# Performance work log

Hardware: AMD Instinct MI355X
Metric: run time of the kernel (lower is better)

The kernel has to match this reference:

```python
import jax, jax.numpy as jnp
import numpy as np

N_FULL = 50000
N_POOL = 12500
E_FULL = 600000
E_POOL = 150000
D = 128


def gcn_conv(x, W, b, edge_index, n):
    """GCNConv with self-loops and symmetric normalization.
    x: [n, d_in], W: [d_in, d_out], edge_index: [2, E] (src -> dst)."""
    xw = x @ W  # [n, d_out]
    loops = jnp.arange(n, dtype=edge_index.dtype)
    src = jnp.concatenate([edge_index[0], loops])
    dst = jnp.concatenate([edge_index[1], loops])
    deg = jnp.zeros((n,), dtype=xw.dtype).at[dst].add(1.0)  # >= 1 (self loops)
    dinv = jax.lax.rsqrt(deg)
    norm = (dinv[src] * dinv[dst])[:, None]  # [E+n, 1]
    out = jax.ops.segment_sum(xw[src] * norm, dst, num_segments=n)
    return out + b


def setup_inputs() -> dict:
    key = jax.random.key(0)
    ks = jax.random.split(key, 8)
    s = 1.0 / np.sqrt(D)
    return {
        "x": jnp.zeros((N_FULL, D), jnp.float32),
        "edge_index": jax.random.randint(ks[0], (2, E_FULL), 0, N_FULL, dtype=jnp.int64)
            if jax.config.jax_enable_x64 else jax.random.randint(ks[0], (2, E_FULL), 0, N_FULL).astype(jnp.int32),
        "pooled_x": jax.random.normal(ks[1], (N_POOL, D), jnp.float32),
        "pooled_edge_index": jax.random.randint(ks[2], (2, E_POOL), 0, N_POOL).astype(jnp.int32),
        "unpool_info": jnp.arange(N_POOL, dtype=jnp.int32),  # unique TopK-kept indices
        "W0": jax.random.normal(ks[3], (D, D), jnp.float32) * s,
        "b0": jnp.zeros((D,), jnp.float32),
        "W1": jax.random.normal(ks[4], (D, D), jnp.float32) * s,
        "b1": jnp.zeros((D,), jnp.float32),
        "W2": jax.random.normal(ks[5], (D, D), jnp.float32) * s,
        "b2": jnp.zeros((D,), jnp.float32),
    }


def reference(x, edge_index, pooled_x, pooled_edge_index, unpool_info,
              W0, b0, W1, b1, W2, b2):
    n = x.shape[0]
    # conv0 on the pooled graph + activation (ELU)
    h = jax.nn.elu(gcn_conv(pooled_x, W0, b0, pooled_edge_index, pooled_x.shape[0]))
    # TopKPool unpool: zero full graph, scatter pooled features to kept indices
    xf = jnp.zeros_like(x).at[unpool_info].set(h)
    # remaining convs on the full graph (dropout=0 / eval mode -> identity)
    xf = jax.nn.elu(gcn_conv(xf, W1, b1, edge_index, n))
    xf = jax.nn.elu(gcn_conv(xf, W2, b2, edge_index, n))
    return xf
```

## Files before the change

### kernel.cpp

```cpp
#include <hip/hip_runtime.h>
#include <math.h>

#define DD 128

static inline int cdiv(long a, long b){ return (int)((a + b - 1) / b); }

__device__ __forceinline__ unsigned bfpack(float a, float b){
  unsigned ua = __float_as_uint(a), ub = __float_as_uint(b);
  ua = (ua + 0x7fffu + ((ua >> 16) & 1u)) >> 16;
  ub = (ub + 0x7fffu + ((ub >> 16) & 1u)) >> 16;
  return ua | (ub << 16);
}

__global__ void k_count2(const int* __restrict__ dst_f, int Ef, int* __restrict__ cnt_f,
                         int* __restrict__ rank_f,
                         const int* __restrict__ dst_p, int Ep, int* __restrict__ cnt_p,
                         int* __restrict__ rank_p,
                         int* __restrict__ invm, int nf){
  int e = blockIdx.x * blockDim.x + threadIdx.x;
  if (e < Ef){ rank_f[e] = atomicAdd(&cnt_f[dst_f[e]], 1); return; }
  e -= Ef;
  if (e < Ep){ rank_p[e] = atomicAdd(&cnt_p[dst_p[e]], 1); return; }
  e -= Ep;
  if (e < nf) invm[e] = -1;
}

__global__ __launch_bounds__(256) void k_bsum(
    const int* __restrict__ cnt_f, int nf, const int* __restrict__ cnt_p, int np,
    int* __restrict__ bsum_f, int* __restrict__ bsum_p, int nbf, int nbp,
    const int* __restrict__ unpool, int* __restrict__ inv, int npool){
  int bi = blockIdx.x;
  if (bi >= nbf + nbp){
    int i = (bi - nbf - nbp) * 256 + threadIdx.x;
    if (i < npool) inv[unpool[i]] = i;
    return;
  }
  const int* cnt; int n; int* bsum; int b;
  if (bi < nbf){ cnt = cnt_f; n = nf; bsum = bsum_f; b = bi; }
  else         { cnt = cnt_p; n = np; bsum = bsum_p; b = bi - nbf; }
  __shared__ int s[256];
  int t = threadIdx.x;
  long base = (long)b * 1024 + t * 4;
  int v = 0;
  if (base + 3 < n){ int4 q = *(const int4*)(cnt + base); v = q.x + q.y + q.z + q.w; }
  else { for (int j = 0; j < 4; j++) if (base + j < n) v += cnt[base + j]; }
  s[t] = v; __syncthreads();
  for (int off = 128; off > 0; off >>= 1){ if (t < off) s[t] += s[t + off]; __syncthreads(); }
  if (t == 0) bsum[b] = s[0];
}

__global__ __launch_bounds__(128) void k_scan_b(int* __restrict__ bsum_f, int nbf,
                                                int* __restrict__ bsum_p, int nbp){
  __shared__ int s[128];
  int t = threadIdx.x;
  int v = (t < nbf) ? bsum_f[t] : 0;
  s[t] = v; __syncthreads();
  for (int off = 1; off < 128; off <<= 1){ int u = (t >= off) ? s[t - off] : 0; __syncthreads(); s[t] += u; __syncthreads(); }
  if (t < nbf) bsum_f[t] = s[t] - v;
  __syncthreads();
  int v2 = (t < nbp) ? bsum_p[t] : 0;
  s[t] = v2; __syncthreads();
  for (int off = 1; off < 128; off <<= 1){ int u = (t >= off) ? s[t - off] : 0; __syncthreads(); s[t] += u; __syncthreads(); }
  if (t < nbp) bsum_p[t] = s[t] - v2;
}

__global__ __launch_bounds__(256) void k_scan_f(
    const int* __restrict__ cnt_f, int nf, const int* __restrict__ bsum_f,
    const int* __restrict__ cnt_p, int np, const int* __restrict__ bsum_p,
    int* __restrict__ rptr_f, float* __restrict__ dinv_f,
    int* __restrict__ rptr_p, float* __restrict__ dinv_p,
    int nbf, int Ef, int Ep){
  const int* cnt; const int* bsum; int* rptr; float* dinv; int n; int b;
  if ((int)blockIdx.x < nbf){ cnt=cnt_f; bsum=bsum_f; rptr=rptr_f; dinv=dinv_f; n=nf; b=blockIdx.x; }
  else                      { cnt=cnt_p; bsum=bsum_p; rptr=rptr_p; dinv=dinv_p; n=np; b=blockIdx.x-nbf; }
  __shared__ int s[256];
  int t = threadIdx.x;
  long base = (long)b * 1024 + t * 4;
  int c0=0,c1=0,c2=0,c3=0;
  if (base + 3 < n){ int4 q = *(const int4*)(cnt + base); c0=q.x; c1=q.y; c2=q.z; c3=q.w; }
  else {
    if (base + 0 < n) c0 = cnt[base + 0];
    if (base + 1 < n) c1 = cnt[base + 1];
    if (base + 2 < n) c2 = cnt[base + 2];
  }
  int tsum = c0 + c1 + c2 + c3;
  s[t] = tsum; __syncthreads();
  for (int off = 1; off < 256; off <<= 1){ int u = (t >= off) ? s[t - off] : 0; __syncthreads(); s[t] += u; __syncthreads(); }
  int run = bsum[b] + s[t] - tsum;
  int r0 = run, r1 = r0 + c0, r2 = r1 + c1, r3 = r2 + c2;
  if (base + 3 < n){
    *(int4*)(rptr + base) = make_int4(r0, r1, r2, r3);
    dinv[base + 0] = rsqrtf((float)(c0 + 1));
    dinv[base + 1] = rsqrtf((float)(c1 + 1));
    dinv[base + 2] = rsqrtf((float)(c2 + 1));
    dinv[base + 3] = rsqrtf((float)(c3 + 1));
  } else {
    if (base + 0 < n){ rptr[base+0]=r0; dinv[base+0]=rsqrtf((float)(c0+1)); }
    if (base + 1 < n){ rptr[base+1]=r1; dinv[base+1]=rsqrtf((float)(c1+1)); }
    if (base + 2 < n){ rptr[base+2]=r2; dinv[base+2]=rsqrtf((float)(c2+1)); }
  }
  if (blockIdx.x == 0 && t == 0){ rptr_f[nf] = Ef; rptr_p[np] = Ep; }
}

__global__ void k_fill2(const int* __restrict__ src_f, const int* __restrict__ dst_f, int Ef,
                        const int* __restrict__ rptr_f, const int* __restrict__ rank_f,
                        int4* __restrict__ ewk_f,
                        const float* __restrict__ dinv_f, const int* __restrict__ inv,
                        const int* __restrict__ src_p, const int* __restrict__ dst_p, int Ep,
                        const int* __restrict__ rptr_p, const int* __restrict__ rank_p,
                        int2* __restrict__ ewk_p,
                        const float* __restrict__ dinv_p){
  int e = blockIdx.x * blockDim.x + threadIdx.x;
  if (e < Ef){
    int s = src_f[e];
    int p = rptr_f[dst_f[e]] + rank_f[e];
    ewk_f[p] = make_int4(s, inv[s], __float_as_int(dinv_f[s]), 0);
  } else {
    e -= Ef;
    if (e < Ep){
      int s = src_p[e];
      int p = rptr_p[dst_p[e]] + rank_p[e];
      ewk_p[p] = make_int2(s, __float_as_int(dinv_p[s]));
    }
  }
}

template <bool BF16OUT>
__global__ __launch_bounds__(256) void k_gemm_t(const float* __restrict__ A,
                                                const float* __restrict__ W,
                                                void* __restrict__ Cout, int n){
  __shared__ float As[16][132];
  __shared__ float Ws[16][128];
  const int t    = threadIdx.x;
  const int row0 = blockIdx.x * 128;
  const int tc   = t & 15;
  const int tr   = t >> 4;
  const int sr   = t >> 2;
  const int sq   = (t & 3) * 4;
  const int wr   = t >> 4;
  const int wq   = (t & 15) * 4;

  float acc[8][8];
  #pragma unroll
  for (int i = 0; i < 8; i++)
    #pragma unroll
    for (int j = 0; j < 8; j++) acc[i][j] = 0.f;

  for (int kt = 0; kt < 128; kt += 16){
    float4 a0 = make_float4(0.f,0.f,0.f,0.f), a1 = a0;
    int r0 = row0 + sr, r1 = row0 + sr + 64;
    if (r0 < n) a0 = *(const float4*)(A + (long)r0 * DD + kt + sq);
    if (r1 < n) a1 = *(const float4*)(A + (long)r1 * DD + kt + sq);
    const float4 wv0 = *(const float4*)(W + (long)(kt + wr) * DD + wq);
    const float4 wv1 = *(const float4*)(W + (long)(kt + wr) * DD + wq + 64);
    __syncthreads();
    As[sq + 0][sr]      = a0.x;  As[sq + 1][sr]      = a0.y;
    As[sq + 2][sr]      = a0.z;  As[sq + 3][sr]      = a0.w;
    As[sq + 0][sr + 64] = a1.x;  As[sq + 1][sr + 64] = a1.y;
    As[sq + 2][sr + 64] = a1.z;  As[sq + 3][sr + 64] = a1.w;
    *(float4*)(&Ws[wr][wq])      = wv0;
    *(float4*)(&Ws[wr][wq + 64]) = wv1;
    __syncthreads();
    #pragma unroll
    for (int k = 0; k < 16; k++){
      const float4 af0 = *(const float4*)(&As[k][tr * 8]);
      const float4 af1 = *(const float4*)(&As[k][tr * 8 + 4]);
      const float4 wf0 = *(const float4*)(&Ws[k][tc * 8]);
      const float4 wf1 = *(const float4*)(&Ws[k][tc * 8 + 4]);
      const float ar[8] = {af0.x,af0.y,af0.z,af0.w,af1.x,af1.y,af1.z,af1.w};
      const float wv[8] = {wf0.x,wf0.y,wf0.z,wf0.w,wf1.x,wf1.y,wf1.z,wf1.w};
      #pragma unroll
      for (int i = 0; i < 8; i++)
        #pragma unroll
        for (int j = 0; j < 8; j++)
          acc[i][j] += ar[i] * wv[j];
    }
  }
  if (BF16OUT){
    unsigned short* C = (unsigned short*)Cout;
    #pragma unroll
    for (int i = 0; i < 8; i++){
      int row = row0 + tr * 8 + i;
      if (row < n){
        uint4 pk;
        pk.x = bfpack(acc[i][0], acc[i][1]);
        pk.y = bfpack(acc[i][2], acc[i][3]);
        pk.z = bfpack(acc[i][4], acc[i][5]);
        pk.w = bfpack(acc[i][6], acc[i][7]);
        *(uint4*)(C + (long)row * DD + tc * 8) = pk;
      }
    }
  } else {
    float* C = (float*)Cout;
    #pragma unroll
    for (int i = 0; i < 8; i++){
      int row = row0 + tr * 8 + i;
      if (row < n){
        *(float4*)(C + (long)row * DD + tc * 8)     = make_float4(acc[i][0], acc[i][1], acc[i][2], acc[i][3]);
        *(float4*)(C + (long)row * DD + tc * 8 + 4) = make_float4(acc[i][4], acc[i][5], acc[i][6], acc[i][7]);
      }
    }
  }
}

__global__ __launch_bounds__(256) void k_agg_csr(const float* __restrict__ xw,
    const int* __restrict__ rptr, const int2* __restrict__ ewk,
    const float* __restrict__ dinv, const float* __restrict__ b,
    float* __restrict__ out, int n){
  int row = blockIdx.x * 4 + (threadIdx.x >> 6);
  if (row >= n) return;
  int c = (threadIdx.x & 63) * 2;
  int j0 = __builtin_amdgcn_readfirstlane(rptr[row]);
  int j1 = __builtin_amdgcn_readfirstlane(rptr[row + 1]);
  float ax[4], ay[4];
  #pragma unroll
  for (int i = 0; i < 4; i++){ ax[i] = 0.f; ay[i] = 0.f; }
  int j = j0;
  for (; j + 3 < j1; j += 4){
    #pragma unroll
    for (int i = 0; i < 4; i++){
      int2 q = ewk[j + i];
      float w = __int_as_float(q.y);
      float2 v = *(const float2*)(xw + (long)q.x * DD + c);
      ax[i] += v.x * w; ay[i] += v.y * w;
    }
  }
  for (; j < j1; j++){
    int2 q = ewk[j];
    float w = __int_as_float(q.y);
    float2 v = *(const float2*)(xw + (long)q.x * DD + c);
    ax[0] += v.x * w; ay[0] += v.y * w;
  }
  float sax = (ax[0]+ax[1]) + (ax[2]+ax[3]);
  float say = (ay[0]+ay[1]) + (ay[2]+ay[3]);
  float dd = dinv[row];
  float2 sv = *(const float2*)(xw + (long)row * DD + c);
  float2 bb = *(const float2*)(b + c);
  float vx = sax * dd + sv.x * dd * dd + bb.x;
  float vy = say * dd + sv.y * dd * dd + bb.y;
  vx = vx > 0.f ? vx : expm1f(vx);
  vy = vy > 0.f ? vy : expm1f(vy);
  *(float2*)(out + (long)row * DD + c) = make_float2(vx, vy);
}

__global__ __launch_bounds__(256) void k_agg_csr_b(const unsigned short* __restrict__ xwb,
    const int* __restrict__ rptr, const int4* __restrict__ ewk,
    const float* __restrict__ dinv, const float* __restrict__ b,
    float* __restrict__ out, int n){
  int row = blockIdx.x * 4 + (threadIdx.x >> 6);
  if (row >= n) return;
  int c = (threadIdx.x & 63) * 2;
  int j0 = __builtin_amdgcn_readfirstlane(rptr[row]);
  int j1 = __builtin_amdgcn_readfirstlane(rptr[row + 1]);
  float ax[8], ay[8];
  #pragma unroll
  for (int i = 0; i < 8; i++){ ax[i] = 0.f; ay[i] = 0.f; }
  int j = j0;
  for (; j + 7 < j1; j += 8){
    #pragma unroll
    for (int i = 0; i < 8; i++){
      int4 q = ewk[j + i];
      float w = __int_as_float(q.z);
      unsigned v = *(const unsigned*)(xwb + (long)q.x * DD + c);
      ax[i] += __uint_as_float(v << 16) * w;
      ay[i] += __uint_as_float(v & 0xffff0000u) * w;
    }
  }
  for (; j < j1; j++){
    int4 q = ewk[j];
    float w = __int_as_float(q.z);
    unsigned v = *(const unsigned*)(xwb + (long)q.x * DD + c);
    ax[0] += __uint_as_float(v << 16) * w;
    ay[0] += __uint_as_float(v & 0xffff0000u) * w;
  }
  float sax = ((ax[0]+ax[1])+(ax[2]+ax[3])) + ((ax[4]+ax[5])+(ax[6]+ax[7]));
  float say = ((ay[0]+ay[1])+(ay[2]+ay[3])) + ((ay[4]+ay[5])+(ay[6]+ay[7]));
  float dd = dinv[row];
  unsigned sv = *(const unsigned*)(xwb + (long)row * DD + c);
  float sx = __uint_as_float(sv << 16), sy = __uint_as_float(sv & 0xffff0000u);
  float2 bb = *(const float2*)(b + c);
  float vx = sax * dd + sx * dd * dd + bb.x;
  float vy = say * dd + sy * dd * dd + bb.y;
  vx = vx > 0.f ? vx : expm1f(vx);
  vy = vy > 0.f ? vy : expm1f(vy);
  *(float2*)(out + (long)row * DD + c) = make_float2(vx, vy);
}

__global__ __launch_bounds__(256) void k_agg_csr_sp_b(const unsigned short* __restrict__ hwb,
    const int* __restrict__ inv, const int* __restrict__ rptr,
    const int4* __restrict__ ewk,
    const float* __restrict__ dinv, const float* __restrict__ b,
    float* __restrict__ out, int n){
  int row = blockIdx.x * 4 + (threadIdx.x >> 6);
  if (row >= n) return;
  int c = (threadIdx.x & 63) * 2;
  int j0 = __builtin_amdgcn_readfirstlane(rptr[row]);
  int j1 = __builtin_amdgcn_readfirstlane(rptr[row + 1]);
  float ax[8], ay[8];
  #pragma unroll
  for (int i = 0; i < 8; i++){ ax[i] = 0.f; ay[i] = 0.f; }
  int j = j0;
  for (; j + 7 < j1; j += 8){
    #pragma unroll
    for (int i = 0; i < 8; i++){
      int4 q = ewk[j + i];
      float w = __int_as_float(q.z);
      if (q.y >= 0){
        unsigned v = *(const unsigned*)(hwb + (long)q.y * DD + c);
        ax[i] += __uint_as_float(v << 16) * w;
        ay[i] += __uint_as_float(v & 0xffff0000u) * w;
      }
    }
  }
  for (; j < j1; j++){
    int4 q = ewk[j];
    float w = __int_as_float(q.z);
    if (q.y >= 0){
      unsigned v = *(const unsigned*)(hwb + (long)q.y * DD + c);
      ax[0] += __uint_as_float(v << 16) * w;
      ay[0] += __uint_as_float(v & 0xffff0000u) * w;
    }
  }
  float sax = ((ax[0]+ax[1])+(ax[2]+ax[3])) + ((ax[4]+ax[5])+(ax[6]+ax[7]));
  float say = ((ay[0]+ay[1])+(ay[2]+ay[3])) + ((ay[4]+ay[5])+(ay[6]+ay[7]));
  float dd = dinv[row];
  int pr = inv[row];
  float sx = 0.f, sy = 0.f;
  if (pr >= 0){
    unsigned sv = *(const unsigned*)(hwb + (long)pr * DD + c);
    sx = __uint_as_float(sv << 16); sy = __uint_as_float(sv & 0xffff0000u);
  }
  float2 bb = *(const float2*)(b + c);
  float vx = sax * dd + sx * dd * dd + bb.x;
  float vy = say * dd + sy * dd * dd + bb.y;
  vx = vx > 0.f ? vx : expm1f(vx);
  vy = vy > 0.f ? vy : expm1f(vy);
  *(float2*)(out + (long)row * DD + c) = make_float2(vx, vy);
}

extern "C" void kernel_launch(void* const* d_in, const int* in_sizes, int n_in,
                              void* d_out, int out_size, void* d_ws, size_t ws_size,
                              hipStream_t stream) {
  const int*   edge   = (const int*)d_in[1];
  const float* px     = (const float*)d_in[2];
  const int*   pedge  = (const int*)d_in[3];
  const int*   unpool = (const int*)d_in[4];
  const float* W0 = (const float*)d_in[5]; const float* b0 = (const float*)d_in[6];
  const float* W1 = (const float*)d_in[7]; const float* b1 = (const float*)d_in[8];
  const float* W2 = (const float*)d_in[9]; const float* b2 = (const float*)d_in[10];
  const int n_full = in_sizes[0] / DD;
  const int E_full = in_sizes[1] / 2;
  const int n_pool = in_sizes[2] / DD;
  const int E_pool = in_sizes[3] / 2;
  float* out = (float*)d_out;

  char* w = (char*)d_ws;
  size_t off = 0;
  auto alloc = [&](size_t bytes) -> void* {
    void* p = (void*)(w + off);
    off += (bytes + 255) / 256 * 256;
    return p;
  };
  float* dinv_p = (float*)alloc((size_t)n_pool * 4);
  float* dinv_f = (float*)alloc((size_t)n_full * 4);
  int* cnt_p  = (int*)alloc((size_t)n_pool * 4);
  int* cnt_f  = (int*)alloc((size_t)n_full * 4);
  size_t cnt_span = (size_t)((char*)(cnt_f + n_full) - (char*)cnt_p);
  int* rptr_p = (int*)alloc((size_t)(n_pool + 1) * 4);
  int* rptr_f = (int*)alloc((size_t)(n_full + 1) * 4);
  int* rank_p = (int*)alloc((size_t)E_pool * 4);
  int* rank_f = (int*)alloc((size_t)E_full * 4);
  int2* ewk_p = (int2*)alloc((size_t)E_pool * 8);
  int4* ewk_f = (int4*)alloc((size_t)E_full * 16);
  int* invm   = (int*)alloc((size_t)n_full * 4);
  const int nbf = cdiv(n_full, 1024), nbp = cdiv(n_pool, 1024);
  int* bsum_f = (int*)alloc((size_t)nbf * 4);
  int* bsum_p = (int*)alloc((size_t)nbp * 4);
  const size_t big = (size_t)n_full * DD * 4;
  float* bufA = (float*)alloc(big);
  float* bufB = (float*)alloc(big);

  const int* src_f = edge;          const int* dst_f = edge + E_full;
  const int* src_p = pedge;         const int* dst_p = pedge + E_pool;

  (void)hipMemsetAsync(cnt_p, 0, cnt_span, stream);
  k_count2<<<cdiv((long)E_full + E_pool + n_full,256),256,0,stream>>>(
      dst_f, E_full, cnt_f, rank_f, dst_p, E_pool, cnt_p, rank_p, invm, n_full);
  const int nbi = cdiv(n_pool, 256);
  k_bsum<<<nbf + nbp + nbi,256,0,stream>>>(cnt_f, n_full, cnt_p, n_pool, bsum_f, bsum_p,
                                           nbf, nbp, unpool, invm, n_pool);
  k_scan_b<<<1,128,0,stream>>>(bsum_f, nbf, bsum_p, nbp);
  k_scan_f<<<nbf + nbp,256,0,stream>>>(cnt_f, n_full, bsum_f, cnt_p, n_pool, bsum_p,
                                       rptr_f, dinv_f, rptr_p, dinv_p,
                                       nbf, E_full, E_pool);
  k_fill2<<<cdiv((long)E_full + E_pool,256),256,0,stream>>>(
      src_f, dst_f, E_full, rptr_f, rank_f, ewk_f, dinv_f, invm,
      src_p, dst_p, E_pool, rptr_p, rank_p, ewk_p, dinv_p);

  float* xw0 = bufA;
  float* h0  = bufB;
  unsigned short* hw1b = (unsigned short*)bufA;
  float* y1  = bufB;
  unsigned short* xw2b = (unsigned short*)bufA;


  k_gemm_t<false><<<cdiv(n_pool,128),256,0,stream>>>(px, W0, xw0, n_pool);
  k_agg_csr<<<cdiv(n_pool,4),256,0,stream>>>(xw0, rptr_p, ewk_p, dinv_p, b0, h0, n_pool);

  k_gemm_t<true><<<cdiv(n_pool,128),256,0,stream>>>(h0, W1, hw1b, n_pool);
  k_agg_csr_sp_b<<<cdiv(n_full,4),256,0,stream>>>(hw1b, invm, rptr_f, ewk_f, dinv_f, b1, y1, n_full);

  k_gemm_t<true><<<cdiv(n_full,128),256,0,stream>>>(y1, W2, xw2b, n_full);
  k_agg_csr_b<<<cdiv(n_full,4),256,0,stream>>>(xw2b, rptr_f, ewk_f, dinv_f, b2, out, n_full);
}
```

Before: 297.8 us.

## Use split-bf16 MFMA GEMM and split edge records into two int2 arrays

Replaces the fp32 SIMT tiled GEMM with an MFMA 16x16x32 bf16 kernel. It splits both A and W into high and low bf16 parts and runs three products to keep near-fp32 accuracy, with W held in swizzled LDS. It also splits the 16-byte full-graph edge records into two 8-byte int2 arrays, one per aggregation kernel, to halve edge-metadata traffic during aggregation. The trade-off is extra MFMA work and conversion overhead, plus scalar, less coalesced output stores.

Result: faster. 285.1 us (-4.3%).

```diff
diff --git a/kernel.cpp b/kernel.cpp
--- a/kernel.cpp
+++ b/kernel.cpp
@@ -5,11 +5,14 @@
 
 static inline int cdiv(long a, long b){ return (int)((a + b - 1) / b); }
 
-__device__ __forceinline__ unsigned bfpack(float a, float b){
-  unsigned ua = __float_as_uint(a), ub = __float_as_uint(b);
-  ua = (ua + 0x7fffu + ((ua >> 16) & 1u)) >> 16;
-  ub = (ub + 0x7fffu + ((ub >> 16) & 1u)) >> 16;
-  return ua | (ub << 16);
+typedef __attribute__((ext_vector_type(4))) float f32x4;
+typedef __attribute__((ext_vector_type(8))) short bf16x8;
+typedef __attribute__((ext_vector_type(4))) short sh4;
+
+__device__ __forceinline__ unsigned short bf16_rn(float f){
+  unsigned u = __float_as_uint(f);
+  u += 0x7fffu + ((u >> 16) & 1u);
+  return (unsigned short)(u >> 16);
 }
 
 __global__ void k_count2(const int* __restrict__ dst_f, int Ef, int* __restrict__ cnt_f,
@@ -104,7 +107,7 @@
 
 __global__ void k_fill2(const int* __restrict__ src_f, const int* __restrict__ dst_f, int Ef,
                         const int* __restrict__ rptr_f, const int* __restrict__ rank_f,
-                        int4* __restrict__ ewk_f,
+                        int2* __restrict__ ewk1_f, int2* __restrict__ ewk2_f,
                         const float* __restrict__ dinv_f, const int* __restrict__ inv,
                         const int* __restrict__ src_p, const int* __restrict__ dst_p, int Ep,
                         const int* __restrict__ rptr_p, const int* __restrict__ rank_p,
@@ -114,7 +117,9 @@
   if (e < Ef){
     int s = src_f[e];
     int p = rptr_f[dst_f[e]] + rank_f[e];
-    ewk_f[p] = make_int4(s, inv[s], __float_as_int(dinv_f[s]), 0);
+    int w = __float_as_int(dinv_f[s]);
+    ewk2_f[p] = make_int2(s, w);
+    ewk1_f[p] = make_int2(inv[s], w);
   } else {
     e -= Ef;
     if (e < Ep){
@@ -126,78 +131,111 @@
 }
 
 template <bool BF16OUT>
-__global__ __launch_bounds__(256) void k_gemm_t(const float* __restrict__ A,
-                                                const float* __restrict__ W,
-                                                void* __restrict__ Cout, int n){
-  __shared__ float As[16][132];
-  __shared__ float Ws[16][128];
+__global__ __launch_bounds__(256, 2) void k_gemm_mfma(const float* __restrict__ A,
+                                                      const float* __restrict__ W,
+                                                      void* __restrict__ Cout, int n){
+  __shared__ unsigned short Wl[2][16384];
   const int t    = threadIdx.x;
-  const int row0 = blockIdx.x * 128;
-  const int tc   = t & 15;
-  const int tr   = t >> 4;
-  const int sr   = t >> 2;
-  const int sq   = (t & 3) * 4;
-  const int wr   = t >> 4;
-  const int wq   = (t & 15) * 4;
-
-  float acc[8][8];
-  #pragma unroll
-  for (int i = 0; i < 8; i++)
-    #pragma unroll
-    for (int j = 0; j < 8; j++) acc[i][j] = 0.f;
-
-  for (int kt = 0; kt < 128; kt += 16){
-    float4 a0 = make_float4(0.f,0.f,0.f,0.f), a1 = a0;
-    int r0 = row0 + sr, r1 = row0 + sr + 64;
-    if (r0 < n) a0 = *(const float4*)(A + (long)r0 * DD + kt + sq);
-    if (r1 < n) a1 = *(const float4*)(A + (long)r1 * DD + kt + sq);
-    const float4 wv0 = *(const float4*)(W + (long)(kt + wr) * DD + wq);
-    const float4 wv1 = *(const float4*)(W + (long)(kt + wr) * DD + wq + 64);
-    __syncthreads();
-    As[sq + 0][sr]      = a0.x;  As[sq + 1][sr]      = a0.y;
-    As[sq + 2][sr]      = a0.z;  As[sq + 3][sr]      = a0.w;
-    As[sq + 0][sr + 64] = a1.x;  As[sq + 1][sr + 64] = a1.y;
-    As[sq + 2][sr + 64] = a1.z;  As[sq + 3][sr + 64] = a1.w;
-    *(float4*)(&Ws[wr][wq])      = wv0;
-    *(float4*)(&Ws[wr][wq + 64]) = wv1;
-    __syncthreads();
-    #pragma unroll
-    for (int k = 0; k < 16; k++){
-      const float4 af0 = *(const float4*)(&As[k][tr * 8]);
-      const float4 af1 = *(const float4*)(&As[k][tr * 8 + 4]);
-      const float4 wf0 = *(const float4*)(&Ws[k][tc * 8]);
-      const float4 wf1 = *(const float4*)(&Ws[k][tc * 8 + 4]);
-      const float ar[8] = {af0.x,af0.y,af0.z,af0.w,af1.x,af1.y,af1.z,af1.w};
-      const float wv[8] = {wf0.x,wf0.y,wf0.z,wf0.w,wf1.x,wf1.y,wf1.z,wf1.w};
+  const int lane = t & 63;
+  const int wv   = t >> 6;
+  const int g    = lane >> 4;
+  const int r    = lane & 15;
+
+  #pragma unroll
+  for (int i = 0; i < 4; i++){
+    int item = t + i * 256;
+    int kq = item >> 5;
+    int c4 = item & 31;
+    const float* Wp = W + (long)kq * 512 + c4 * 4;
+    float4 ww[4];
+    #pragma unroll
+    for (int kk = 0; kk < 4; kk++) ww[kk] = *(const float4*)(Wp + kk * 128);
+    #pragma unroll
+    for (int m = 0; m < 4; m++){
+      int c = c4 * 4 + m;
+      int boff = c * 256 + (((kq >> 1) ^ (c & 15)) * 16) + (kq & 1) * 8;
+      sh4 hq, lq;
       #pragma unroll
-      for (int i = 0; i < 8; i++)
-        #pragma unroll
-        for (int j = 0; j < 8; j++)
-          acc[i][j] += ar[i] * wv[j];
-    }
-  }
-  if (BF16OUT){
-    unsigned short* C = (unsigned short*)Cout;
-    #pragma unroll
-    for (int i = 0; i < 8; i++){
-      int row = row0 + tr * 8 + i;
-      if (row < n){
-        uint4 pk;
-        pk.x = bfpack(acc[i][0], acc[i][1]);
-        pk.y = bfpack(acc[i][2], acc[i][3]);
-        pk.z = bfpack(acc[i][4], acc[i][5]);
-        pk.w = bfpack(acc[i][6], acc[i][7]);
-        *(uint4*)(C + (long)row * DD + tc * 8) = pk;
+      for (int kk = 0; kk < 4; kk++){
+        float f = ((const float*)&ww[kk])[m];
+        unsigned short hh = bf16_rn(f);
+        float hf = __uint_as_float((unsigned)hh << 16);
+        hq[kk] = (short)hh;
+        lq[kk] = (short)bf16_rn(f - hf);
       }
-    }
-  } else {
-    float* C = (float*)Cout;
-    #pragma unroll
-    for (int i = 0; i < 8; i++){
-      int row = row0 + tr * 8 + i;
-      if (row < n){
-        *(float4*)(C + (long)row * DD + tc * 8)     = make_float4(acc[i][0], acc[i][1], acc[i][2], acc[i][3]);
-        *(float4*)(C + (long)row * DD + tc * 8 + 4) = make_float4(acc[i][4], acc[i][5], acc[i][6], acc[i][7]);
+      *(sh4*)((char*)(&Wl[0][0]) + boff) = hq;
+      *(sh4*)((char*)(&Wl[1][0]) + boff) = lq;
+    }
+  }
+  __syncthreads();
+
+  const int rb = blockIdx.x * 128 + wv * 32;
+  const int r0 = rb + r, r1 = rb + 16 + r;
+  const bool v0 = r0 < n, v1 = r1 < n;
+  const float* pa0 = A + (long)r0 * DD + g * 8;
+  const float* pa1 = A + (long)r1 * DD + g * 8;
+
+  f32x4 acc[2][8];
+  #pragma unroll
+  for (int i = 0; i < 2; i++)
+    #pragma unroll
+    for (int j = 0; j < 8; j++){ f32x4 z = {0.f,0.f,0.f,0.f}; acc[i][j] = z; }
+
+  #pragma unroll
+  for (int ks = 0; ks < 4; ks++){
+    const float4 z4 = make_float4(0.f,0.f,0.f,0.f);
+    float4 a00 = v0 ? *(const float4*)(pa0 + ks * 32)     : z4;
+    float4 a01 = v0 ? *(const float4*)(pa0 + ks * 32 + 4) : z4;
+    float4 a10 = v1 ? *(const float4*)(pa1 + ks * 32)     : z4;
+    float4 a11 = v1 ? *(const float4*)(pa1 + ks * 32 + 4) : z4;
+    bf16x8 ah0, al0, ah1, al1;
+    {
+      float f[8] = {a00.x,a00.y,a00.z,a00.w,a01.x,a01.y,a01.z,a01.w};
+      #pragma unroll
+      for (int i = 0; i < 8; i++){
+        unsigned short hh = bf16_rn(f[i]);
+        ah0[i] = (short)hh;
+        al0[i] = (short)bf16_rn(f[i] - __uint_as_float((unsigned)hh << 16));
+      }
+    }
+    {
+      float f[8] = {a10.x,a10.y,a10.z,a10.w,a11.x,a11.y,a11.z,a11.w};
+      #pragma unroll
+      for (int i = 0; i < 8; i++){
+        unsigned short hh = bf16_rn(f[i]);
+        ah1[i] = (short)hh;
+        al1[i] = (short)bf16_rn(f[i] - __uint_as_float((unsigned)hh << 16));
+      }
+    }
+    const int sb = ks * 4 + g;
+    #pragma unroll
+    for (int cf = 0; cf < 8; cf++){
+      const int boff = (cf * 16 + r) * 256 + ((sb ^ r) * 16);
+      bf16x8 wh = *(const bf16x8*)((const char*)(&Wl[0][0]) + boff);
+      bf16x8 wl = *(const bf16x8*)((const char*)(&Wl[1][0]) + boff);
+      acc[0][cf] = __builtin_amdgcn_mfma_f32_16x16x32_bf16(ah0, wh, acc[0][cf], 0, 0, 0);
+      acc[1][cf] = __builtin_amdgcn_mfma_f32_16x16x32_bf16(ah1, wh, acc[1][cf], 0, 0, 0);
+      acc[0][cf] = __builtin_amdgcn_mfma_f32_16x16x32_bf16(al0, wh, acc[0][cf], 0, 0, 0);
+      acc[1][cf] = __builtin_amdgcn_mfma_f32_16x16x32_bf16(al1, wh, acc[1][cf], 0, 0, 0);
+      acc[0][cf] = __builtin_amdgcn_mfma_f32_16x16x32_bf16(ah0, wl, acc[0][cf], 0, 0, 0);
+      acc[1][cf] = __builtin_amdgcn_mfma_f32_16x16x32_bf16(ah1, wl, acc[1][cf], 0, 0, 0);
+    }
+  }
+
+  #pragma unroll
+  for (int rf = 0; rf < 2; rf++){
+    #pragma unroll
+    for (int cf = 0; cf < 8; cf++){
+      #pragma unroll
+      for (int e = 0; e < 4; e++){
+        int row = rb + rf * 16 + g * 4 + e;
+        if (row < n){
+          float v = acc[rf][cf][e];
+          if (BF16OUT)
+            ((unsigned short*)Cout)[(long)row * DD + cf * 16 + r] = bf16_rn(v);
+          else
+            ((float*)Cout)[(long)row * DD + cf * 16 + r] = v;
+        }
       }
     }
   }
@@ -244,7 +282,7 @@
 }
 
 __global__ __launch_bounds__(256) void k_agg_csr_b(const unsigned short* __restrict__ xwb,
-    const int* __restrict__ rptr, const int4* __restrict__ ewk,
+    const int* __restrict__ rptr, const int2* __restrict__ ewk,
     const float* __restrict__ dinv, const float* __restrict__ b,
     float* __restrict__ out, int n){
   int row = blockIdx.x * 4 + (threadIdx.x >> 6);
@@ -259,16 +297,16 @@
   for (; j + 7 < j1; j += 8){
     #pragma unroll
     for (int i = 0; i < 8; i++){
-      int4 q = ewk[j + i];
-      float w = __int_as_float(q.z);
+      int2 q = ewk[j + i];
+      float w = __int_as_float(q.y);
       unsigned v = *(const unsigned*)(xwb + (long)q.x * DD + c);
       ax[i] += __uint_as_float(v << 16) * w;
       ay[i] += __uint_as_float(v & 0xffff0000u) * w;
     }
   }
   for (; j < j1; j++){
-    int4 q = ewk[j];
-    float w = __int_as_float(q.z);
+    int2 q = ewk[j];
+    float w = __int_as_float(q.y);
     unsigned v = *(const unsigned*)(xwb + (long)q.x * DD + c);
     ax[0] += __uint_as_float(v << 16) * w;
     ay[0] += __uint_as_float(v & 0xffff0000u) * w;
@@ -288,7 +326,7 @@
 
 __global__ __launch_bounds__(256) void k_agg_csr_sp_b(const unsigned short* __restrict__ hwb,
     const int* __restrict__ inv, const int* __restrict__ rptr,
-    const int4* __restrict__ ewk,
+    const int2* __restrict__ ewk,
     const float* __restrict__ dinv, const float* __restrict__ b,
     float* __restrict__ out, int n){
   int row = blockIdx.x * 4 + (threadIdx.x >> 6);
@@ -303,20 +341,20 @@
   for (; j + 7 < j1; j += 8){
     #pragma unroll
     for (int i = 0; i < 8; i++){
-      int4 q = ewk[j + i];
-      float w = __int_as_float(q.z);
-      if (q.y >= 0){
-        unsigned v = *(const unsigned*)(hwb + (long)q.y * DD + c);
+      int2 q = ewk[j + i];
+      float w = __int_as_float(q.y);
+      if (q.x >= 0){
+        unsigned v = *(const unsigned*)(hwb + (long)q.x * DD + c);
         ax[i] += __uint_as_float(v << 16) * w;
         ay[i] += __uint_as_float(v & 0xffff0000u) * w;
       }
     }
   }
   for (; j < j1; j++){
-    int4 q = ewk[j];
-    float w = __int_as_float(q.z);
-    if (q.y >= 0){
-      unsigned v = *(const unsigned*)(hwb + (long)q.y * DD + c);
+    int2 q = ewk[j];
+    float w = __int_as_float(q.y);
+    if (q.x >= 0){
+      unsigned v = *(const unsigned*)(hwb + (long)q.x * DD + c);
       ax[0] += __uint_as_float(v << 16) * w;
       ay[0] += __uint_as_float(v & 0xffff0000u) * w;
     }
@@ -370,8 +408,9 @@
   int* rptr_f = (int*)alloc((size_t)(n_full + 1) * 4);
   int* rank_p = (int*)alloc((size_t)E_pool * 4);
   int* rank_f = (int*)alloc((size_t)E_full * 4);
-  int2* ewk_p = (int2*)alloc((size_t)E_pool * 8);
-  int4* ewk_f = (int4*)alloc((size_t)E_full * 16);
+  int2* ewk_p  = (int2*)alloc((size_t)E_pool * 8);
+  int2* ewk1_f = (int2*)alloc((size_t)E_full * 8);
+  int2* ewk2_f = (int2*)alloc((size_t)E_full * 8);
   int* invm   = (int*)alloc((size_t)n_full * 4);
   const int nbf = cdiv(n_full, 1024), nbp = cdiv(n_pool, 1024);
   int* bsum_f = (int*)alloc((size_t)nbf * 4);
@@ -394,7 +433,7 @@
                                        rptr_f, dinv_f, rptr_p, dinv_p,
                                        nbf, E_full, E_pool);
   k_fill2<<<cdiv((long)E_full + E_pool,256),256,0,stream>>>(
-      src_f, dst_f, E_full, rptr_f, rank_f, ewk_f, dinv_f, invm,
+      src_f, dst_f, E_full, rptr_f, rank_f, ewk1_f, ewk2_f, dinv_f, invm,
       src_p, dst_p, E_pool, rptr_p, rank_p, ewk_p, dinv_p);
 
   float* xw0 = bufA;
@@ -403,13 +442,12 @@
   float* y1  = bufB;
   unsigned short* xw2b = (unsigned short*)bufA;
 
-
-  k_gemm_t<false><<<cdiv(n_pool,128),256,0,stream>>>(px, W0, xw0, n_pool);
+  k_gemm_mfma<false><<<cdiv(n_pool,128),256,0,stream>>>(px, W0, xw0, n_pool);
   k_agg_csr<<<cdiv(n_pool,4),256,0,stream>>>(xw0, rptr_p, ewk_p, dinv_p, b0, h0, n_pool);
 
-  k_gemm_t<true><<<cdiv(n_pool,128),256,0,stream>>>(h0, W1, hw1b, n_pool);
-  k_agg_csr_sp_b<<<cdiv(n_full,4),256,0,stream>>>(hw1b, invm, rptr_f, ewk_f, dinv_f, b1, y1, n_full);
-
-  k_gemm_t<true><<<cdiv(n_full,128),256,0,stream>>>(y1, W2, xw2b, n_full);
-  k_agg_csr_b<<<cdiv(n_full,4),256,0,stream>>>(xw2b, rptr_f, ewk_f, dinv_f, b2, out, n_full);
-}
+  k_gemm_mfma<true><<<cdiv(n_pool,128),256,0,stream>>>(h0, W1, hw1b, n_pool);
+  k_agg_csr_sp_b<<<cdiv(n_full,4),256,0,stream>>>(hw1b, invm, rptr_f, ewk1_f, dinv_f, b1, y1, n_full);
+
+  k_gemm_mfma<true><<<cdiv(n_full,128),256,0,stream>>>(y1, W2, xw2b, n_full);
+  k_agg_csr_b<<<cdiv(n_full,4),256,0,stream>>>(xw2b, rptr_f, ewk2_f, dinv_f, b2, out, n_full);
+}
```
